# Optimization experiments

Measured on AMD Instinct MI355X. Metric: run time of the kernel, lower is better.

The kernel has to match this reference:

```python
import jax, jax.numpy as jnp
import numpy as np

SIZE = 84        # pupil size
SIZE_F = 167     # field grid size
X_PAD = 39       # pad for 90 -> 167
KNUM = 16        # number of phase kernels (== required batch size)
CENTER = 120     # center crop
NOISE = 0.003


def _disk_mask(M=SIZE, R=SIZE / 2.0):
    # get_amp: unit disk of radius R on an MxM grid
    x, y = np.meshgrid(np.arange(-(M - 1) / 2, M / 2), np.arange(-(M - 1) / 2, M / 2))
    return jnp.asarray((x ** 2 + y ** 2 <= R ** 2).astype(np.float32))


def setup_inputs() -> dict:
    key = jax.random.key(0)
    k1, k2, k3 = jax.random.split(key, 3)
    x = jax.random.uniform(k1, (16, 90, 90, 1), dtype=jnp.float32)
    P = jax.random.uniform(k2, (16, 84, 84), dtype=jnp.float32,
                           minval=-0.5 * np.pi, maxval=0.5 * np.pi)
    W3 = jax.random.normal(k3, (12800, 10), dtype=jnp.float32) * 0.01
    b3 = jnp.zeros((10,), dtype=jnp.float32)
    return {"x": x, "P": P, "W3": W3, "b3": b3}


def _forward(x, P, W3, b3):
    mask = _disk_mask()
    amp = jnp.sum(mask)  # normalization of the autocorrelation

    # --- input field: pad 90 -> 167, complex, fftshift/fft2/fftshift ---
    # NOTE: tf.signal.fftshift default shifts ALL axes (incl. batch); the two
    # shifts cancel on the batch axis, replicated faithfully here.
    xp = jnp.pad(x, ((0, 0), (X_PAD, X_PAD - 1), (X_PAD, X_PAD - 1), (0, 0)))[..., 0]
    xc = xp.astype(jnp.complex64)
    X = jnp.fft.fftshift(jnp.fft.fft2(jnp.fft.fftshift(xc)))  # [16,167,167]
    Xr = jnp.repeat(X, KNUM, axis=0)                          # [256,167,167]

    # --- OTF: FFT-accelerated autocorrelation of the pupil P_amp*exp(i*phase) ---
    Pc = (mask * jnp.cos(P) + 1j * mask * jnp.sin(P)).astype(jnp.complex64)  # [16,84,84]
    Pp = jnp.pad(Pc, ((0, 0), (42, 41), (42, 41)))                           # [16,167,167]
    F = jnp.fft.fft2(Pp)
    OTF = jnp.fft.fftshift(jnp.fft.ifft2(F * jnp.conj(F)))  # all-axes shift
    OTF = jnp.concatenate([OTF[8:], OTF[:8]], axis=0) / amp  # undoes batch roll

    # --- propagation: multiply in frequency domain, back to space ---
    y = Xr * jnp.tile(OTF, (KNUM, 1, 1))  # [256,167,167]
    y = jnp.fft.fftshift(jnp.fft.ifft2(jnp.fft.fftshift(y)))
    r = jnp.real(y).reshape(16, KNUM, SIZE_F, SIZE_F)
    # per image: kernels 0..7 minus kernels 8..15 -> channels
    d = jnp.transpose(r[:, :8] - r[:, 8:], (0, 2, 3, 1))  # [16,167,167,8]

    # additive noise (np.random in original; fixed key -> deterministic constant)
    d = d + NOISE * jax.random.normal(jax.random.key(42), d.shape, dtype=jnp.float32)

    # center crop, relu, 3x3/3 max-pool, flatten, softmax dense
    b = (SIZE_F + 1) // 2 - CENTER // 2  # 24
    c = jax.nn.relu(d[:, b:b + CENTER, b:b + CENTER, :])  # [16,120,120,8]
    pooled = jax.lax.reduce_window(c, -jnp.inf, jax.lax.max,
                                   (1, 3, 3, 1), (1, 3, 3, 1), 'VALID')  # [16,40,40,8]
    flat = pooled.reshape(16, -1)  # [16,12800]
    return jax.nn.softmax(flat @ W3 + b3)


def reference(x, P, W3, b3):
    return _forward(x, P, W3, b3)
```

## Files before the change

kernel.cpp:

```cpp
#include <hip/hip_runtime.h>
#include <math.h>

constexpr int N  = 167;
constexpr int NN = 167 * 167;
constexpr int NP = 90;
constexpr int MP = 84;
constexpr int CROP = 120;
constexpr int HCOL = 84;
constexpr int HALF_SZ = 1784896;

constexpr size_t SZ_MAT   = (size_t)NN * 2;
constexpr size_t OFF_M1   = 0;
constexpr size_t OFF_M1T  = OFF_M1 + SZ_MAT;
constexpr size_t OFF_WF   = OFF_M1T + SZ_MAT;
constexpr size_t OFF_M2   = OFF_WF + SZ_MAT;
constexpr size_t OFF_M2T  = OFF_M2 + SZ_MAT;
constexpr size_t OFF_M3   = OFF_M2T + SZ_MAT;
constexpr size_t OFF_M3T84= OFF_M3 + (size_t)CROP * N * 2;
constexpr size_t OFF_PHI2 = OFF_M3T84 + (size_t)HCOL * CROP * 2;
constexpr size_t OFF_AMP  = OFF_PHI2 + (size_t)N * 2;
constexpr size_t OFF_X    = OFF_AMP + 4;
constexpr size_t OFF_T1   = OFF_X  + (size_t)16 * N * HCOL * 2;
constexpr size_t OFF_A    = OFF_T1 + (size_t)16 * N * NP * 2;
constexpr size_t OFF_T2   = OFF_A  + (size_t)16 * NN * 2;
constexpr size_t OFF_BD   = OFF_T2 + (size_t)16 * N * MP * 2;
constexpr size_t OFF_T3   = OFF_BD + (size_t)8 * NN;
constexpr size_t OFF_OTF  = OFF_T3 + (size_t)8 * N * HCOL * 2;
constexpr size_t OFF_FLAT = OFF_OTF+ (size_t)8 * N * HCOL * 2;
constexpr size_t OFF_PC   = OFF_FLAT + (size_t)16 * 12800;
constexpr size_t WS_FLOATS = OFF_PC + (size_t)16 * MP * MP * 2;

__device__ __forceinline__ unsigned rotl32(unsigned x, int r) {
    return (x << r) | (x >> (32 - r));
}

__device__ float noise_at(unsigned idx) {
    unsigned c0, c1; int lane;
    if (idx < (unsigned)HALF_SZ) { c0 = idx; c1 = idx + HALF_SZ; lane = 0; }
    else                         { c0 = idx - HALF_SZ; c1 = idx; lane = 1; }
    const unsigned ks0 = 0u, ks1 = 42u, ks2 = 0x1BD11BDAu ^ 42u;
    unsigned x0 = c0 + ks0, x1 = c1 + ks1;
#define TFR(r) { x0 += x1; x1 = rotl32(x1, r); x1 ^= x0; }
    TFR(13) TFR(15) TFR(26) TFR(6)   x0 += ks1; x1 += ks2 + 1u;
    TFR(17) TFR(29) TFR(16) TFR(24)  x0 += ks2; x1 += ks0 + 2u;
    TFR(13) TFR(15) TFR(26) TFR(6)   x0 += ks0; x1 += ks1 + 3u;
    TFR(17) TFR(29) TFR(16) TFR(24)  x0 += ks1; x1 += ks2 + 4u;
    TFR(13) TFR(15) TFR(26) TFR(6)   x0 += ks2; x1 += ks0 + 5u;
#undef TFR
    unsigned bits = lane ? x1 : x0;
    float u01 = __uint_as_float((bits >> 9) | 0x3F800000u) - 1.0f;
    const float lo = -0.99999994f;
    float f = fmaxf(lo, u01 * 2.0f + lo);
    float w = -log1pf(-f * f);
    float p;
    if (w < 5.0f) {
        w -= 2.5f;
        p = 2.81022636e-08f;
        p = fmaf(p, w, 3.43273939e-07f);
        p = fmaf(p, w, -3.5233877e-06f);
        p = fmaf(p, w, -4.39150654e-06f);
        p = fmaf(p, w, 0.00021858087f);
        p = fmaf(p, w, -0.00125372503f);
        p = fmaf(p, w, -0.00417768164f);
        p = fmaf(p, w, 0.246640727f);
        p = fmaf(p, w, 1.50140941f);
    } else {
        w = sqrtf(w) - 3.0f;
        p = -0.000200214257f;
        p = fmaf(p, w, 0.000100950558f);
        p = fmaf(p, w, 0.00134934322f);
        p = fmaf(p, w, -0.00367342844f);
        p = fmaf(p, w, 0.00573950773f);
        p = fmaf(p, w, -0.0076224613f);
        p = fmaf(p, w, 0.00943887047f);
        p = fmaf(p, w, 1.00167406f);
        p = fmaf(p, w, 2.83297682f);
    }
    return 1.41421356237f * p * f;
}

__global__ void k_prep(const float* __restrict__ P, float* ws) {
    int bx = blockIdx.x, t = threadIdx.x;
    if (bx < 109) {
        __shared__ float2 wtab[N];
        const float TPI = (float)(6.283185307179586476925286766559 / 167.0);
        for (int i = t; i < N; i += 256) {
            float s, c; sincosf(TPI * (float)i, &s, &c);
            wtab[i] = make_float2(c, s);
        }
        __syncthreads();
        int id = bx * 256 + t;
        if (id >= NN) return;
        int k = id / N, m = id % N;
        const float inv = 1.0f / 167.0f;
        int t1 = ((k + 84) * ((m + 83) % N)) % N;
        float2 w1 = wtab[t1];
        ws[OFF_M1 + 2 * id] = w1.x;  ws[OFF_M1 + 2 * id + 1] = -w1.y;
        ws[OFF_M1T + 2 * (m * N + k)] = w1.x;  ws[OFF_M1T + 2 * (m * N + k) + 1] = -w1.y;
        int tw = (k * m) % N;
        float2 ww = wtab[tw];
        ws[OFF_WF + 2 * id] = ww.x;  ws[OFF_WF + 2 * id + 1] = -ww.y;
        int t2 = ((k + 84) * m) % N;
        float2 w2 = wtab[t2];
        ws[OFF_M2 + 2 * id] = w2.x * inv;  ws[OFF_M2 + 2 * id + 1] = w2.y * inv;
        ws[OFF_M2T + 2 * (m * N + k)] = w2.x * inv;  ws[OFF_M2T + 2 * (m * N + k) + 1] = w2.y * inv;
        if (k < CROP) {
            int t3 = ((k + 108) * ((m + 83) % N)) % N;
            float2 w3 = wtab[t3];
            ws[OFF_M3 + 2 * (k * N + m)] = w3.x * inv;  ws[OFF_M3 + 2 * (k * N + m) + 1] = w3.y * inv;
            if (m < HCOL) {
                ws[OFF_M3T84 + 2 * (m * CROP + k)] = w3.x * inv;
                ws[OFF_M3T84 + 2 * (m * CROP + k) + 1] = w3.y * inv;
            }
        }
        if (id < N) {
            float2 wp = wtab[(2 * id) % N];
            ws[OFF_PHI2 + 2 * id] = wp.x;
            ws[OFF_PHI2 + 2 * id + 1] = wp.y;
        }
    } else if (bx < 550) {
        int id = (bx - 109) * 256 + t;
        if (id >= 16 * MP * MP) return;
        int rc = id % (MP * MP);
        int r = rc / MP, c = rc % MP;
        float y = r - 41.5f, x = c - 41.5f;
        float2 v = {0.f, 0.f};
        if (x * x + y * y <= 1764.0f) {
            float sp, cp; sincosf(P[id], &sp, &cp);
            v.x = cp; v.y = sp;
        }
        ((float2*)(ws + OFF_PC))[id] = v;
    } else {
        __shared__ int red[256];
        int cnt = 0;
        for (int i = t; i < MP * MP; i += 256) {
            int r = i / MP, c = i % MP;
            float y = r - 41.5f, x = c - 41.5f;
            if (x * x + y * y <= 1764.0f) cnt++;
        }
        red[t] = cnt; __syncthreads();
        for (int s = 128; s > 0; s >>= 1) { if (t < s) red[t] += red[t + s]; __syncthreads(); }
        if (t == 0) ws[OFF_AMP] = (float)red[0];
    }
}

__global__ __launch_bounds__(128) void k_rows(const float* __restrict__ x, float* ws) {
    int kr = blockIdx.x, bj = blockIdx.y, t = threadIdx.x;
    __shared__ float2 wbuf[NP];
    if (blockIdx.z == 0) {
        const float2* M1 = (const float2*)(ws + OFF_M1);
        if (t < NP) wbuf[t] = M1[kr * N + 39 + t];
        __syncthreads();
        if (t >= NP) return;
        float2 acc = {0.f, 0.f};
        for (int nr = 0; nr < NP; nr++) {
            float2 w = wbuf[nr];
            float xv = x[(bj * NP + nr) * NP + t];
            acc.x += w.x * xv; acc.y += w.y * xv;
        }
        ((float2*)(ws + OFF_T1))[(bj * N + kr) * NP + t] = acc;
    } else {
        const float2* WF = (const float2*)(ws + OFF_WF);
        if (t < MP) wbuf[t] = WF[kr * N + 42 + t];
        __syncthreads();
        if (t >= MP) return;
        const float2* PC = (const float2*)(ws + OFF_PC) + (size_t)bj * MP * MP;
        float2 acc = {0.f, 0.f};
        for (int nr = 0; nr < MP; nr++) {
            float2 w = wbuf[nr];
            float2 pc = PC[nr * MP + t];
            acc.x += w.x * pc.x - w.y * pc.y;
            acc.y += w.x * pc.y + w.y * pc.x;
        }
        ((float2*)(ws + OFF_T2))[(bj * N + kr) * MP + t] = acc;
    }
}

constexpr int RCH = 6;
__global__ __launch_bounds__(192) void k_cols(float* ws) {
    int bj = blockIdx.y, tid = threadIdx.x;
    __shared__ __align__(16) float2 sbuf[RCH * MP];
    if (blockIdx.x < 84) {
        int k0 = blockIdx.x * 2;
        const float2* T1 = (const float2*)(ws + OFF_T1);
        for (int idx = tid; idx < 2 * NP; idx += 192) {
            int r = idx / NP, m = idx % NP;
            if (k0 + r < N) sbuf[r * NP + m] = T1[((size_t)bj * N + k0 + r) * NP + m];
        }
        __syncthreads();
        int col = tid % HCOL, grp = tid / HCOL;
        if (grp >= 2) return;
        int kr = k0 + grp;
        if (kr >= N) return;
        const float2* M1T = (const float2*)(ws + OFF_M1T);
        float2 acc = {0.f, 0.f};
#pragma unroll 5
        for (int ncp = 0; ncp < 45; ncp++) {
            int nc = 2 * ncp;
            float4 u = *(const float4*)&sbuf[grp * NP + nc];
            float2 w0 = M1T[(39 + nc) * N + col];
            float2 w1 = M1T[(40 + nc) * N + col];
            acc.x += u.x * w0.x - u.y * w0.y;
            acc.y += u.x * w0.y + u.y * w0.x;
            acc.x += u.z * w1.x - u.w * w1.y;
            acc.y += u.z * w1.y + u.w * w1.x;
        }
        ((float2*)(ws + OFF_X))[((size_t)bj * N + kr) * HCOL + col] = acc;
    } else {
        int i0 = (blockIdx.x - 84) * RCH;
        const float2* T2 = (const float2*)(ws + OFF_T2);
        for (int idx = tid; idx < RCH * MP; idx += 192) {
            int q = idx / MP, nc = idx % MP, kr = i0 + q;
            if (kr < N) sbuf[idx] = T2[(bj * N + kr) * MP + nc];
        }
        __syncthreads();
        if (tid >= N) return;
        const float2* WF = (const float2*)(ws + OFF_WF);
        float2 acc[RCH];
#pragma unroll
        for (int q = 0; q < RCH; q++) acc[q] = make_float2(0.f, 0.f);
        for (int ncp = 0; ncp < 42; ncp++) {
            int nc = 2 * ncp;
            float2 w0 = WF[(42 + nc) * N + tid];
            float2 w1 = WF[(43 + nc) * N + tid];
#pragma unroll
            for (int q = 0; q < RCH; q++) {
                float4 u = *(const float4*)&sbuf[q * MP + nc];
                acc[q].x += u.x * w0.x - u.y * w0.y;
                acc[q].y += u.x * w0.y + u.y * w0.x;
                acc[q].x += u.z * w1.x - u.w * w1.y;
                acc[q].y += u.z * w1.y + u.w * w1.x;
            }
        }
        float2* A = (float2*)(ws + OFF_A);
#pragma unroll
        for (int q = 0; q < RCH; q++)
            if (i0 + q < N) A[((size_t)bj * N + i0 + q) * N + tid] = acc[q];
    }
}

__global__ __launch_bounds__(192) void k2c(float* ws) {
    int chunk = blockIdx.x, c = blockIdx.y, tid = threadIdx.x;
    int k0 = chunk * 2;
    __shared__ float bds[2][N];
    const float2* A = (const float2*)(ws + OFF_A);
    float inv_amp = 1.0f / ws[OFF_AMP];
    for (int idx = tid; idx < 2 * N; idx += 192) {
        int r = idx / N, m = idx % N;
        int k = k0 + r;
        if (k < N) {
            float2 a0 = A[((size_t)c * N + k) * N + m];
            float2 a1 = A[((size_t)(c + 8) * N + k) * N + m];
            bds[r][m] = (a0.x * a0.x + a0.y * a0.y - a1.x * a1.x - a1.y * a1.y) * inv_amp;
        }
    }
    __syncthreads();
    int col = tid % HCOL, grp = tid / HCOL;
    if (grp >= 2) return;
    int k = k0 + grp;
    if (k >= N) return;
    const float2* M2T = (const float2*)(ws + OFF_M2T);
    float2 acc = {0.f, 0.f};
    for (int m = 0; m < N; m++) {
        float bv = bds[grp][m];
        float2 w = M2T[m * N + col];
        acc.x += w.x * bv; acc.y += w.y * bv;
    }
    ((float2*)(ws + OFF_T3))[((size_t)c * N + k) * HCOL + col] = acc;
}

__global__ __launch_bounds__(192) void k2d(float* ws) {
    int chunk = blockIdx.x, c = blockIdx.y, tid = threadIdx.x;
    int i0 = chunk * 2;
    __shared__ float2 m2s[2][N];
    const float2* M2 = (const float2*)(ws + OFF_M2);
    for (int idx = tid; idx < 2 * N; idx += 192) {
        int r = idx / N, k = idx % N;
        if (i0 + r < N) m2s[r][k] = M2[(i0 + r) * N + k];
    }
    __syncthreads();
    int col = tid % HCOL, grp = tid / HCOL;
    if (grp >= 2) return;
    int i = i0 + grp;
    if (i >= N) return;
    const float2* T3 = (const float2*)(ws + OFF_T3) + (size_t)c * N * HCOL;
    float2 acc = {0.f, 0.f};
    for (int k = 0; k < N; k++) {
        float2 w = m2s[grp][k];
        float2 u = T3[k * HCOL + col];
        acc.x += u.x * w.x - u.y * w.y;
        acc.y += u.x * w.y + u.y * w.x;
    }
    ((float2*)(ws + OFF_OTF))[((size_t)c * N + i) * HCOL + col] = acc;
}

constexpr int K34R = 12;
constexpr int KCH  = 16;
constexpr int NT34 = (N + KCH - 1) / KCH;

constexpr int SM_ZS   = 0;
constexpr int SM_M3C  = SM_ZS + 2 * KCH * HCOL * 2;
constexpr int SM_PHIS = SM_M3C + 2 * KCH * K34R * 2;
constexpr int SM_PM   = SM_PHIS + N * 2;
constexpr int SM_TOT  = SM_PM + 4 * CROP;

constexpr int ZBUF = KCH * HCOL;
constexpr int MBUF = KCH * K34R;

#define K34_FMA_BODY(kl)                                                        \
    {                                                                           \
        float4 zz = *(const float4*)&zcur[(kl) * HCOL + 2 * pair];              \
        float4 wa = *(const float4*)&mcur[(kl) * K34R + r0];                    \
        a00.x += wa.x * zz.x - wa.y * zz.y;  a00.y += wa.x * zz.y + wa.y * zz.x;\
        a01.x += wa.x * zz.z - wa.y * zz.w;  a01.y += wa.x * zz.w + wa.y * zz.z;\
        a10.x += wa.z * zz.x - wa.w * zz.y;  a10.y += wa.z * zz.y + wa.w * zz.x;\
        a11.x += wa.z * zz.z - wa.w * zz.w;  a11.y += wa.z * zz.w + wa.w * zz.z;\
    }

__global__ __launch_bounds__(256, 8) void k34(float* ws) {
    int chunk = blockIdx.x, c = blockIdx.y, b = blockIdx.z, tid = threadIdx.x;
    int i0 = chunk * K34R;
    __shared__ __align__(16) float smem[SM_TOT];
    float2* zbase = (float2*)(smem + SM_ZS);
    float2* mbase = (float2*)(smem + SM_M3C);
    float2* phis  = (float2*)(smem + SM_PHIS);
    float*  pmf   = smem + SM_PM;
    float2 (*us)[HCOL] = (float2 (*)[HCOL])(smem + SM_ZS);

    const float2* M3 = (const float2*)(ws + OFF_M3);
    const float4* X4   = (const float4*)(ws + OFF_X   + (size_t)b * N * HCOL * 2);
    const float4* OTF4 = (const float4*)(ws + OFF_OTF + (size_t)c * N * HCOL * 2);
    for (int idx = tid; idx < N; idx += 256) phis[idx] = ((const float2*)(ws + OFF_PHI2))[idx];

    int qkl[3], qcp[3];
#pragma unroll
    for (int e = 0; e < 3; e++) {
        int idx = tid + e * 256;
        qkl[e] = idx / 42; qcp[e] = idx - qkl[e] * 42;
    }
    int mkl = tid & 15, mr = tid >> 4;

    int pair = tid % 42, grp = tid / 42;
    int r0 = grp * 2;
    float2 a00 = {0.f,0.f}, a01 = {0.f,0.f}, a10 = {0.f,0.f}, a11 = {0.f,0.f};

    float4 xq[3], oq[3];
    float2 m3r;

#pragma unroll
    for (int e = 0; e < 3; e++)
        if (qkl[e] < KCH) { xq[e] = X4[qkl[e] * 42 + qcp[e]]; oq[e] = OTF4[qkl[e] * 42 + qcp[e]]; }
    if (tid < 192) m3r = M3[(i0 + mr) * N + mkl];
#pragma unroll
    for (int e = 0; e < 3; e++)
        if (qkl[e] < KCH) {
            float4 z;
            z.x = xq[e].x * oq[e].x - xq[e].y * oq[e].y;
            z.y = xq[e].x * oq[e].y + xq[e].y * oq[e].x;
            z.z = xq[e].z * oq[e].z - xq[e].w * oq[e].w;
            z.w = xq[e].z * oq[e].w + xq[e].w * oq[e].z;
            *(float4*)&zbase[qkl[e] * HCOL + 2 * qcp[e]] = z;
        }
    if (tid < 192) mbase[mkl * K34R + mr] = m3r;
    __syncthreads();

    for (int t = 0; t < NT34; t++) {
        int cbuf = t & 1, nbuf = cbuf ^ 1;
        int kr0 = t * KCH;
        int chn = min(KCH, N - kr0);
        int nbase = kr0 + KCH;
        int nchn = (t + 1 < NT34) ? (N - nbase < KCH ? N - nbase : KCH) : 0;
        if (nchn > 0) {
#pragma unroll
            for (int e = 0; e < 3; e++)
                if (qkl[e] < nchn) { xq[e] = X4[(nbase + qkl[e]) * 42 + qcp[e]];
                                     oq[e] = OTF4[(nbase + qkl[e]) * 42 + qcp[e]]; }
            if (tid < 192 && mkl < nchn) m3r = M3[(i0 + mr) * N + nbase + mkl];
        }
        const float2* zcur = zbase + cbuf * ZBUF;
        const float2* mcur = mbase + cbuf * MBUF;
        if (grp < 6) {
            if (chn == KCH) {
#pragma unroll
                for (int kl = 0; kl < KCH; kl++) K34_FMA_BODY(kl)
            } else {
#pragma unroll
                for (int kl = 0; kl < KCH - 9; kl++) K34_FMA_BODY(kl)
            }
        }
        if (nchn > 0) {
            float2* znxt = zbase + nbuf * ZBUF;
            float2* mnxt = mbase + nbuf * MBUF;
#pragma unroll
            for (int e = 0; e < 3; e++)
                if (qkl[e] < nchn) {
                    float4 z;
                    z.x = xq[e].x * oq[e].x - xq[e].y * oq[e].y;
                    z.y = xq[e].x * oq[e].y + xq[e].y * oq[e].x;
                    z.z = xq[e].z * oq[e].z - xq[e].w * oq[e].w;
                    z.w = xq[e].z * oq[e].w + xq[e].w * oq[e].z;
                    *(float4*)&znxt[qkl[e] * HCOL + 2 * qcp[e]] = z;
                }
            if (tid < 192 && mkl < nchn) mnxt[mkl * K34R + mr] = m3r;
        }
        __syncthreads();
    }

    if (grp < 6) {
        *(float4*)&us[r0][2 * pair]     = make_float4(a00.x, a00.y, a01.x, a01.y);
        *(float4*)&us[r0 + 1][2 * pair] = make_float4(a10.x, a10.y, a11.x, a11.y);
    }
    __syncthreads();

    if (tid < 240) {
        int grp2 = tid / CROP, j = tid % CROP;
        int rbase = grp2 * 6;
        const float2* M3T84 = (const float2*)(ws + OFF_M3T84);
        float2 A[6]; float Bq[6];
#pragma unroll
        for (int q = 0; q < 6; q++) A[q] = make_float2(0.f, 0.f);
#pragma unroll 4
        for (int ncp = 0; ncp < 41; ncp++) {
            int nc = 2 * ncp;
            float2 w0 = M3T84[nc * CROP + j];
            float2 w1 = M3T84[(nc + 1) * CROP + j];
#pragma unroll
            for (int q = 0; q < 6; q++) {
                float4 u = *(const float4*)&us[rbase + q][nc];
                A[q].x += u.x * w0.x - u.y * w0.y;
                A[q].y += u.x * w0.y + u.y * w0.x;
                A[q].x += u.z * w1.x - u.w * w1.y;
                A[q].y += u.z * w1.y + u.w * w1.x;
            }
        }
        {
            float2 w = M3T84[82 * CROP + j];
#pragma unroll
            for (int q = 0; q < 6; q++) {
                float2 u = us[rbase + q][82];
                A[q].x += u.x * w.x - u.y * w.y;
                A[q].y += u.x * w.y + u.y * w.x;
            }
        }
        {
            float2 w = M3T84[(HCOL - 1) * CROP + j];
#pragma unroll
            for (int q = 0; q < 6; q++) {
                float2 u = us[rbase + q][HCOL - 1];
                Bq[q] = u.x * w.x - u.y * w.y;
            }
        }
#pragma unroll
        for (int g = 0; g < 2; g++) {
            float vmax = 0.f;
#pragma unroll
            for (int r = 0; r < 3; r++) {
                int q = g * 3 + r, i = i0 + rbase + q;
                int s = i + j + 49; if (s >= N) s -= N;
                float2 ph = phis[s];
                float val = A[q].x * (1.0f + ph.x) - A[q].y * ph.y + Bq[q];
                unsigned idx = (((unsigned)b * N + (24 + i)) * N + (24 + j)) * 8u + c;
                val += 0.003f * noise_at(idx);
                vmax = fmaxf(vmax, val);
            }
            pmf[(grp2 * 2 + g) * CROP + j] = vmax;
        }
    }
    __syncthreads();
    if (tid < 160) {
        int pr = tid / 40, pc = tid % 40;
        float m = fmaxf(fmaxf(pmf[pr * CROP + 3 * pc], pmf[pr * CROP + 3 * pc + 1]),
                        pmf[pr * CROP + 3 * pc + 2]);
        int prow = chunk * 4 + pr;
        ws[OFF_FLAT + (size_t)b * 12800 + ((size_t)prow * 40 + pc) * 8 + c] = m;
    }
}

__global__ void k5(const float* __restrict__ W3, const float* __restrict__ b3,
                   const float* __restrict__ ws, float* __restrict__ out) {
    int b = blockIdx.x, t = threadIdx.x;
    __shared__ float red[256][10];
    float acc[10];
#pragma unroll
    for (int o = 0; o < 10; o++) acc[o] = 0.f;
    const float* fl = ws + OFF_FLAT + (size_t)b * 12800;
    for (int f = t; f < 12800; f += 256) {
        float v = fl[f];
#pragma unroll
        for (int o = 0; o < 10; o++) acc[o] = fmaf(v, W3[f * 10 + o], acc[o]);
    }
#pragma unroll
    for (int o = 0; o < 10; o++) red[t][o] = acc[o];
    __syncthreads();
    for (int s = 128; s > 0; s >>= 1) {
        if (t < s) {
#pragma unroll
            for (int o = 0; o < 10; o++) red[t][o] += red[t + s][o];
        }
        __syncthreads();
    }
    if (t == 0) {
        float lg[10], mx = -1e30f;
#pragma unroll
        for (int o = 0; o < 10; o++) { lg[o] = red[0][o] + b3[o]; mx = fmaxf(mx, lg[o]); }
        float sum = 0.f;
#pragma unroll
        for (int o = 0; o < 10; o++) { lg[o] = expf(lg[o] - mx); sum += lg[o]; }
#pragma unroll
        for (int o = 0; o < 10; o++) out[b * 10 + o] = lg[o] / sum;
    }
}

extern "C" void kernel_launch(void* const* d_in, const int* in_sizes, int n_in,
                              void* d_out, int out_size, void* d_ws, size_t ws_size,
                              hipStream_t stream) {
    const float* x  = (const float*)d_in[0];
    const float* P  = (const float*)d_in[1];
    const float* W3 = (const float*)d_in[2];
    const float* b3 = (const float*)d_in[3];
    float* ws  = (float*)d_ws;
    float* out = (float*)d_out;

    k_prep<<<551, 256, 0, stream>>>(P, ws);
    k_rows<<<dim3(N, 16, 2), 128, 0, stream>>>(x, ws);
    k_cols<<<dim3(84 + 28, 16), 192, 0, stream>>>(ws);
    k2c<<<dim3(84, 8), 192, 0, stream>>>(ws);
    k2d<<<dim3(84, 8), 192, 0, stream>>>(ws);
    k34<<<dim3(CROP / K34R, 8, 16), 256, 0, stream>>>(ws);
    k5<<<16, 256, 0, stream>>>(W3, b3, ws, out);
}
```

Baseline: 204.3 us.

## Use Hermitian symmetry in OTF transform and enlarge k34 per-thread register tile

k2c now computes only half of the 84 output columns and writes the other half as the complex conjugate, which exploits the symmetry of the real-valued input. It also processes four rows per block, halving the grid. k34 drops to 128 threads per block, and each thread accumulates four rows instead of two, so every shared-memory z load is reused across more FMAs. The staging and epilogue loops become strided, and a few inner loops get unroll 2. The changes trade occupancy and parallelism for more register reuse, and the symmetry trick assumes T3 columns are exactly conjugate mirrored.

```diff
diff --git a/kernel.cpp b/kernel.cpp
--- a/kernel.cpp
+++ b/kernel.cpp
@@ -153,6 +153,7 @@
         __syncthreads();
         if (t >= NP) return;
         float2 acc = {0.f, 0.f};
+#pragma unroll 2
         for (int nr = 0; nr < NP; nr++) {
             float2 w = wbuf[nr];
             float xv = x[(bj * NP + nr) * NP + t];
@@ -166,6 +167,7 @@
         if (t >= MP) return;
         const float2* PC = (const float2*)(ws + OFF_PC) + (size_t)bj * MP * MP;
         float2 acc = {0.f, 0.f};
+#pragma unroll 2
         for (int nr = 0; nr < MP; nr++) {
             float2 w = wbuf[nr];
             float2 pc = PC[nr * MP + t];
@@ -241,11 +243,11 @@
 
 __global__ __launch_bounds__(192) void k2c(float* ws) {
     int chunk = blockIdx.x, c = blockIdx.y, tid = threadIdx.x;
-    int k0 = chunk * 2;
-    __shared__ float bds[2][N];
+    int k0 = chunk * 4;
+    __shared__ float bds[4][N];
     const float2* A = (const float2*)(ws + OFF_A);
     float inv_amp = 1.0f / ws[OFF_AMP];
-    for (int idx = tid; idx < 2 * N; idx += 192) {
+    for (int idx = tid; idx < 4 * N; idx += 192) {
         int r = idx / N, m = idx % N;
         int k = k0 + r;
         if (k < N) {
@@ -255,18 +257,21 @@
         }
     }
     __syncthreads();
-    int col = tid % HCOL, grp = tid / HCOL;
-    if (grp >= 2) return;
+    int col = tid % 42, grp = tid / 42;
+    if (grp >= 4) return;
     int k = k0 + grp;
     if (k >= N) return;
     const float2* M2T = (const float2*)(ws + OFF_M2T);
     float2 acc = {0.f, 0.f};
+#pragma unroll 2
     for (int m = 0; m < N; m++) {
         float bv = bds[grp][m];
         float2 w = M2T[m * N + col];
         acc.x += w.x * bv; acc.y += w.y * bv;
     }
-    ((float2*)(ws + OFF_T3))[((size_t)c * N + k) * HCOL + col] = acc;
+    float2* T3 = (float2*)(ws + OFF_T3) + ((size_t)c * N + k) * HCOL;
+    T3[col] = acc;
+    T3[83 - col] = make_float2(acc.x, -acc.y);
 }
 
 __global__ __launch_bounds__(192) void k2d(float* ws) {
@@ -285,6 +290,7 @@
     if (i >= N) return;
     const float2* T3 = (const float2*)(ws + OFF_T3) + (size_t)c * N * HCOL;
     float2 acc = {0.f, 0.f};
+#pragma unroll 2
     for (int k = 0; k < N; k++) {
         float2 w = m2s[grp][k];
         float2 u = T3[k * HCOL + col];
@@ -311,13 +317,18 @@
     {                                                                           \
         float4 zz = *(const float4*)&zcur[(kl) * HCOL + 2 * pair];              \
         float4 wa = *(const float4*)&mcur[(kl) * K34R + r0];                    \
+        float4 wb = *(const float4*)&mcur[(kl) * K34R + r0 + 2];                \
         a00.x += wa.x * zz.x - wa.y * zz.y;  a00.y += wa.x * zz.y + wa.y * zz.x;\
         a01.x += wa.x * zz.z - wa.y * zz.w;  a01.y += wa.x * zz.w + wa.y * zz.z;\
         a10.x += wa.z * zz.x - wa.w * zz.y;  a10.y += wa.z * zz.y + wa.w * zz.x;\
         a11.x += wa.z * zz.z - wa.w * zz.w;  a11.y += wa.z * zz.w + wa.w * zz.z;\
-    }
-
-__global__ __launch_bounds__(256, 8) void k34(float* ws) {
+        a20.x += wb.x * zz.x - wb.y * zz.y;  a20.y += wb.x * zz.y + wb.y * zz.x;\
+        a21.x += wb.x * zz.z - wb.y * zz.w;  a21.y += wb.x * zz.w + wb.y * zz.z;\
+        a30.x += wb.z * zz.x - wb.w * zz.y;  a30.y += wb.z * zz.y + wb.w * zz.x;\
+        a31.x += wb.z * zz.z - wb.w * zz.w;  a31.y += wb.z * zz.w + wb.w * zz.z;\
+    }
+
+__global__ __launch_bounds__(128) void k34(float* ws) {
     int chunk = blockIdx.x, c = blockIdx.y, b = blockIdx.z, tid = threadIdx.x;
     int i0 = chunk * K34R;
     __shared__ __align__(16) float smem[SM_TOT];
@@ -330,29 +341,31 @@
     const float2* M3 = (const float2*)(ws + OFF_M3);
     const float4* X4   = (const float4*)(ws + OFF_X   + (size_t)b * N * HCOL * 2);
     const float4* OTF4 = (const float4*)(ws + OFF_OTF + (size_t)c * N * HCOL * 2);
-    for (int idx = tid; idx < N; idx += 256) phis[idx] = ((const float2*)(ws + OFF_PHI2))[idx];
-
-    int qkl[3], qcp[3];
-#pragma unroll
-    for (int e = 0; e < 3; e++) {
-        int idx = tid + e * 256;
+    for (int idx = tid; idx < N; idx += 128) phis[idx] = ((const float2*)(ws + OFF_PHI2))[idx];
+
+    int qkl[6], qcp[6];
+#pragma unroll
+    for (int e = 0; e < 6; e++) {
+        int idx = tid + e * 128;
         qkl[e] = idx / 42; qcp[e] = idx - qkl[e] * 42;
     }
     int mkl = tid & 15, mr = tid >> 4;
 
-    int pair = tid % 42, grp = tid / 42;
-    int r0 = grp * 2;
+    int pair = tid % 42, quad = tid / 42;
+    int r0 = quad * 4;
     float2 a00 = {0.f,0.f}, a01 = {0.f,0.f}, a10 = {0.f,0.f}, a11 = {0.f,0.f};
-
-    float4 xq[3], oq[3];
-    float2 m3r;
-
-#pragma unroll
-    for (int e = 0; e < 3; e++)
+    float2 a20 = {0.f,0.f}, a21 = {0.f,0.f}, a30 = {0.f,0.f}, a31 = {0.f,0.f};
+
+    float4 xq[6], oq[6];
+    float2 m3r0, m3r1;
+
+#pragma unroll
+    for (int e = 0; e < 6; e++)
         if (qkl[e] < KCH) { xq[e] = X4[qkl[e] * 42 + qcp[e]]; oq[e] = OTF4[qkl[e] * 42 + qcp[e]]; }
-    if (tid < 192) m3r = M3[(i0 + mr) * N + mkl];
-#pragma unroll
-    for (int e = 0; e < 3; e++)
+    m3r0 = M3[(i0 + mr) * N + mkl];
+    if (tid + 128 < 192) m3r1 = M3[(i0 + mr + 8) * N + mkl];
+#pragma unroll
+    for (int e = 0; e < 6; e++)
         if (qkl[e] < KCH) {
             float4 z;
             z.x = xq[e].x * oq[e].x - xq[e].y * oq[e].y;
@@ -361,7 +374,8 @@
             z.w = xq[e].z * oq[e].w + xq[e].w * oq[e].z;
             *(float4*)&zbase[qkl[e] * HCOL + 2 * qcp[e]] = z;
         }
-    if (tid < 192) mbase[mkl * K34R + mr] = m3r;
+    mbase[mkl * K34R + mr] = m3r0;
+    if (tid + 128 < 192) mbase[mkl * K34R + mr + 8] = m3r1;
     __syncthreads();
 
     for (int t = 0; t < NT34; t++) {
@@ -372,14 +386,17 @@
         int nchn = (t + 1 < NT34) ? (N - nbase < KCH ? N - nbase : KCH) : 0;
         if (nchn > 0) {
 #pragma unroll
-            for (int e = 0; e < 3; e++)
+            for (int e = 0; e < 6; e++)
                 if (qkl[e] < nchn) { xq[e] = X4[(nbase + qkl[e]) * 42 + qcp[e]];
                                      oq[e] = OTF4[(nbase + qkl[e]) * 42 + qcp[e]]; }
-            if (tid < 192 && mkl < nchn) m3r = M3[(i0 + mr) * N + nbase + mkl];
+            if (mkl < nchn) {
+                m3r0 = M3[(i0 + mr) * N + nbase + mkl];
+                if (tid + 128 < 192) m3r1 = M3[(i0 + mr + 8) * N + nbase + mkl];
+            }
         }
         const float2* zcur = zbase + cbuf * ZBUF;
         const float2* mcur = mbase + cbuf * MBUF;
-        if (grp < 6) {
+        if (quad < 3) {
             if (chn == KCH) {
 #pragma unroll
                 for (int kl = 0; kl < KCH; kl++) K34_FMA_BODY(kl)
@@ -392,7 +409,7 @@
             float2* znxt = zbase + nbuf * ZBUF;
             float2* mnxt = mbase + nbuf * MBUF;
 #pragma unroll
-            for (int e = 0; e < 3; e++)
+            for (int e = 0; e < 6; e++)
                 if (qkl[e] < nchn) {
                     float4 z;
                     z.x = xq[e].x * oq[e].x - xq[e].y * oq[e].y;
@@ -401,19 +418,24 @@
                     z.w = xq[e].z * oq[e].w + xq[e].w * oq[e].z;
                     *(float4*)&znxt[qkl[e] * HCOL + 2 * qcp[e]] = z;
                 }
-            if (tid < 192 && mkl < nchn) mnxt[mkl * K34R + mr] = m3r;
-        }
-        __syncthreads();
-    }
-
-    if (grp < 6) {
+            if (mkl < nchn) {
+                mnxt[mkl * K34R + mr] = m3r0;
+                if (tid + 128 < 192) mnxt[mkl * K34R + mr + 8] = m3r1;
+            }
+        }
+        __syncthreads();
+    }
+
+    if (quad < 3) {
         *(float4*)&us[r0][2 * pair]     = make_float4(a00.x, a00.y, a01.x, a01.y);
         *(float4*)&us[r0 + 1][2 * pair] = make_float4(a10.x, a10.y, a11.x, a11.y);
+        *(float4*)&us[r0 + 2][2 * pair] = make_float4(a20.x, a20.y, a21.x, a21.y);
+        *(float4*)&us[r0 + 3][2 * pair] = make_float4(a30.x, a30.y, a31.x, a31.y);
     }
     __syncthreads();
 
-    if (tid < 240) {
-        int grp2 = tid / CROP, j = tid % CROP;
+    for (int jt = tid; jt < 240; jt += 128) {
+        int grp2 = jt / CROP, j = jt % CROP;
         int rbase = grp2 * 6;
         const float2* M3T84 = (const float2*)(ws + OFF_M3T84);
         float2 A[6]; float Bq[6];
@@ -467,8 +489,8 @@
         }
     }
     __syncthreads();
-    if (tid < 160) {
-        int pr = tid / 40, pc = tid % 40;
+    for (int idx = tid; idx < 160; idx += 128) {
+        int pr = idx / 40, pc = idx % 40;
         float m = fmaxf(fmaxf(pmf[pr * CROP + 3 * pc], pmf[pr * CROP + 3 * pc + 1]),
                         pmf[pr * CROP + 3 * pc + 2]);
         int prow = chunk * 4 + pr;
@@ -524,8 +546,8 @@
     k_prep<<<551, 256, 0, stream>>>(P, ws);
     k_rows<<<dim3(N, 16, 2), 128, 0, stream>>>(x, ws);
     k_cols<<<dim3(84 + 28, 16), 192, 0, stream>>>(ws);
-    k2c<<<dim3(84, 8), 192, 0, stream>>>(ws);
+    k2c<<<dim3(42, 8), 192, 0, stream>>>(ws);
     k2d<<<dim3(84, 8), 192, 0, stream>>>(ws);
-    k34<<<dim3(CROP / K34R, 8, 16), 256, 0, stream>>>(ws);
+    k34<<<dim3(CROP / K34R, 8, 16), 128, 0, stream>>>(ws);
     k5<<<16, 256, 0, stream>>>(W3, b3, ws, out);
 }
```

Result: slower. 307.8 us (+50.6%).
